# Kernel tuning notes

Measured on AMD Instinct MI355X. Metric: run time of the kernel, lower is better.

The kernel has to match this reference:

```python
import jax, jax.numpy as jnp
import numpy as np

N_ORDERS = 2
CHUNK = 64            # real tokens per chunk
LINEAR_ACTIVATION = False
STAB = 10000.0


def _ensure_stability(x):
    x = jnp.clip(x, -STAB, STAB)
    return jnp.nan_to_num(x, nan=0.0, posinf=STAB, neginf=-STAB)


def setup_inputs() -> dict:
    key = jax.random.key(0)
    k1, k2, k3, k4 = jax.random.split(key, 4)
    B, H, NC, D = 2, 16, 32, 128
    CT = CHUNK * N_ORDERS  # 128 virtual tokens per chunk
    s = 1.0 / np.sqrt(D)
    q_chunks = jax.random.normal(k1, (B, H, NC, CT, D), jnp.float32) * s
    W = jax.random.normal(k2, (B, H, NC, CT, D), jnp.float32) * s
    U = jax.random.normal(k3, (B, H, NC, CT, D), jnp.float32) * s
    h0 = jax.random.normal(k4, (B, H, D, D), jnp.float32) * s
    return {"q_chunks": q_chunks, "W": W, "U": U, "h0": h0}


def _gelu_norm(h):
    # h_norm/2 * gelu(2*h/h_norm, tanh) applied to chunk-boundary state
    n = jnp.linalg.norm(h, axis=-1, keepdims=True) + 1e-6
    return n / 2.0 * jax.nn.gelu(2.0 * h / n, approximate=True)


def _delta_product_scan(q_chunks, W, U, h0):
    B, H, NC, CT, D = q_chunks.shape
    C = CT // N_ORDERS

    def body(h, chunk):
        q_c, w_c, u_c = chunk  # each [B,H,CT,D]
        # virtual-token layout: token c, step s lives at index c*n_orders+s
        qs = q_c.reshape(B, H, C, N_ORDERS, D)
        ws = w_c.reshape(B, H, C, N_ORDERS, D)
        us = u_c.reshape(B, H, C, N_ORDERS, D)
        state = jnp.broadcast_to(h[:, :, None], (B, H, C, D, D))  # per-token state
        outs = []
        for step in range(N_ORDERS):
            q_s = qs[:, :, :, step]
            w_s = ws[:, :, :, step]
            u_s = us[:, :, :, step]
            k_trans_h = jnp.einsum('bhcd,bhcde->bhce', w_s, state)
            u_val = u_s - k_trans_h
            o_inter = jnp.einsum('bhcd,bhcde->bhce', q_s, state)
            o_intra = q_s * u_val  # elementwise, as in source
            outs.append(o_intra + o_inter)
            state = _ensure_stability(state + w_s[..., :, None] * u_val[..., None, :])
        out = jnp.stack(outs, axis=3).reshape(B, H, CT, D)
        h_new = state[:, :, -1]
        if not LINEAR_ACTIVATION:
            h_new = _gelu_norm(h_new)
        return h_new, out

    chunks = (jnp.moveaxis(q_chunks, 2, 0), jnp.moveaxis(W, 2, 0), jnp.moveaxis(U, 2, 0))
    h_final, ys = jax.lax.scan(body, h0, chunks)
    return jnp.moveaxis(ys, 0, 2), h_final  # [B,H,NC,CT,D], [B,H,D,D]


def reference(q_chunks, W, U, h0):
    return _delta_product_scan(q_chunks, W, U, h0)
```

## Files before the change

kernel.cpp:

```cpp
#include <hip/hip_runtime.h>


#define Dd 128
#define NCH 32
#define YS 16777216

typedef __attribute__((ext_vector_type(4))) float floatx4;
typedef __attribute__((ext_vector_type(8))) short short8;

__device__ __forceinline__ unsigned cvtpk(float lo, float hi) {
  unsigned r;
  asm("v_cvt_pk_bf16_f32 %0, %1, %2" : "=v"(r) : "v"(lo), "v"(hi));
  return r;
}

__global__ __launch_bounds__(512) void p1_scan(const float* __restrict__ W,
    const float* __restrict__ U, const float* __restrict__ h0,
    unsigned short* __restrict__ hws, float* __restrict__ out) {
  __shared__ float wpre[NCH * 320];
  __shared__ float upre[NCH * 2 * Dd];
  __shared__ float d10pre[NCH];
  __shared__ float sqb[Dd * 129];
  __shared__ float nrm2[4 * 40];

  const int bh = blockIdx.x;
  const int t = threadIdx.x;
  const int w = t >> 6, l = t & 63;
  const int c = (w << 4) | (l & 15);
  const int rg = l >> 4;

  {
    const float* Wg = W + (size_t)bh * NCH * 16384;
    const float* Ug = U + (size_t)bh * NCH * 16384;
#pragma unroll
    for (int k = 0; k < 4; k++) {
      int idx4 = k * 512 + t;
      int n = idx4 >> 6;
      int rem = idx4 & 63;
      int r = rem >> 5, e4 = (rem & 31) * 4;
      size_t g = (size_t)n * 16384 + (size_t)(126 + r) * Dd + e4;
      *(float4*)&upre[idx4 * 4] = *(const float4*)&Ug[g];
      *(float4*)&wpre[n * 320 + r * 160 + (e4 >> 5) * 40 + (e4 & 31)] =
          *(const float4*)&Wg[g];
    }
  }
  {
    const float4* hg = (const float4*)(h0 + (size_t)bh * 16384);
#pragma unroll
    for (int k = 0; k < 8; k++) {
      int idx4 = k * 512 + t;
      float4 v = hg[idx4];
      int d = idx4 >> 5, e4 = (idx4 & 31) * 4;
      sqb[d * 129 + e4 + 0] = v.x;
      sqb[d * 129 + e4 + 1] = v.y;
      sqb[d * 129 + e4 + 2] = v.z;
      sqb[d * 129 + e4 + 3] = v.w;
    }
  }
  __syncthreads();
  {
    int n = t >> 4, j = t & 15;
    const float* w0p = &wpre[n * 320 + (j >> 2) * 40 + (j & 3) * 8];
    const float* w1p = w0p + 160;
    float p = 0.f;
#pragma unroll
    for (int i = 0; i < 8; i++) p += w0p[i] * w1p[i];
    p += __shfl_xor(p, 1, 64);
    p += __shfl_xor(p, 2, 64);
    p += __shfl_xor(p, 4, 64);
    p += __shfl_xor(p, 8, 64);
    if (j == 0) d10pre[n] = p;
  }
  float hr[32];
#pragma unroll
  for (int i = 0; i < 32; i++) hr[i] = sqb[(rg * 32 + i) * 129 + c];
  __syncthreads();

  const int cpos = (c & 96) | ((c + 8 * rg) & 31);
  float* sqw = &sqb[rg * 32 * 129 + cpos];
  const int srow = t >> 2, sst = t & 3;
  const float* sqr = &sqb[srow * 129 + sst * 32];

  unsigned short* hwsb = hws + (size_t)bh * NCH * 16384;
  {
    unsigned pk[16];
#pragma unroll
    for (int i = 0; i < 16; i++) pk[i] = cvtpk(hr[2 * i], hr[2 * i + 1]);
    uint4* dst = (uint4*)(hwsb + (size_t)c * Dd + rg * 32);
    dst[0] = make_uint4(pk[0], pk[1], pk[2], pk[3]);
    dst[1] = make_uint4(pk[4], pk[5], pk[6], pk[7]);
    dst[2] = make_uint4(pk[8], pk[9], pk[10], pk[11]);
    dst[3] = make_uint4(pk[12], pk[13], pk[14], pk[15]);
  }

  for (int n = 0; n < NCH; n++) {
    floatx4 w0v[8], w1v[8];
    const float* wb = &wpre[n * 320 + rg * 40];
#pragma unroll
    for (int i = 0; i < 8; i++) {
      w0v[i] = *(const floatx4*)&wb[4 * i];
      w1v[i] = *(const floatx4*)&wb[160 + 4 * i];
    }
    float a0 = 0.f, a1 = 0.f, b0 = 0.f, b1 = 0.f;
#pragma unroll
    for (int i = 0; i < 8; i += 2) {
#pragma unroll
      for (int j = 0; j < 4; j++) {
        float h0v = hr[4 * i + j];
        float h1v = hr[4 * i + 4 + j];
        a0 = fmaf(w0v[i][j], h0v, a0);
        a1 = fmaf(w1v[i][j], h0v, a1);
        b0 = fmaf(w0v[i + 1][j], h1v, b0);
        b1 = fmaf(w1v[i + 1][j], h1v, b1);
      }
    }
    a0 += b0; a1 += b1;
    a0 += __shfl_xor(a0, 16, 64);
    a0 += __shfl_xor(a0, 32, 64);
    a1 += __shfl_xor(a1, 16, 64);
    a1 += __shfl_xor(a1, 32, 64);
    const float u0 = upre[n * 256 + c];
    const float u1 = upre[n * 256 + Dd + c];
    const float d10 = d10pre[n];
    const float uv0 = u0 - a0;
    const float uv1 = u1 - a1 - d10 * uv0;
#pragma unroll
    for (int i = 0; i < 8; i++)
#pragma unroll
      for (int j = 0; j < 4; j++) {
        int ii = 4 * i + j;
        float s = __builtin_amdgcn_fmed3f(fmaf(w0v[i][j], uv0, hr[ii]),
                                          -10000.0f, 10000.0f);
        s = __builtin_amdgcn_fmed3f(fmaf(w1v[i][j], uv1, s),
                                    -10000.0f, 10000.0f);
        hr[ii] = s;
        sqw[ii * 129] = s;
      }
    __syncthreads();
    {
      float acc = 0.f, acc2 = 0.f;
#pragma unroll
      for (int b = 0; b < 4; b++) {
        const float* p = sqr + 8 * ((b + sst) & 3);
#pragma unroll
        for (int i = 0; i < 8; i += 2) {
          float v = p[i], v2 = p[i + 1];
          acc = fmaf(v, v, acc);
          acc2 = fmaf(v2, v2, acc2);
        }
      }
      acc += acc2;
      acc += __shfl_xor(acc, 1, 64);
      acc += __shfl_xor(acc, 2, 64);
      if (sst == 0) {
        float nd = sqrtf(acc) + 1e-6f;
        nrm2[(srow >> 5) * 40 + (srow & 31)] = __fdividef(2.0f, nd);
      }
    }
    __syncthreads();
    floatx4 r2v[8];
    const float* nb = &nrm2[rg * 40];
#pragma unroll
    for (int i = 0; i < 8; i++) r2v[i] = *(const floatx4*)&nb[4 * i];
#pragma unroll
    for (int i = 0; i < 8; i++)
#pragma unroll
      for (int j = 0; j < 4; j++) {
        int ii = 4 * i + j;
        float h = hr[ii];
        float x = h * r2v[i][j];
        float x2 = x * x;
        float aa = x * fmaf(0.071354816f, x2, 1.59576912f);
        float ex = __expf(-aa);
        hr[ii] = __fdividef(h, 1.0f + ex);
      }
    if (n < NCH - 1) {
      unsigned pk[16];
#pragma unroll
      for (int i = 0; i < 16; i++) pk[i] = cvtpk(hr[2 * i], hr[2 * i + 1]);
      uint4* dst = (uint4*)(hwsb + (size_t)(n + 1) * 16384 + (size_t)c * Dd + rg * 32);
      dst[0] = make_uint4(pk[0], pk[1], pk[2], pk[3]);
      dst[1] = make_uint4(pk[4], pk[5], pk[6], pk[7]);
      dst[2] = make_uint4(pk[8], pk[9], pk[10], pk[11]);
      dst[3] = make_uint4(pk[12], pk[13], pk[14], pk[15]);
    } else {
      float* ob = out + YS + (size_t)bh * 16384;
#pragma unroll
      for (int i = 0; i < 32; i++) ob[(rg * 32 + i) * Dd + c] = hr[i];
    }
  }
}


__device__ __forceinline__ void stage_slice(const float* Qb, const float* Wb,
    float* qd, float* wd, int kc, int wv6, int ln) {
#pragma unroll
  for (int i = 0; i < 4; i++) {
    int cb = i * 512 + wv6 * 64;
    int isW = cb >> 10;
    int cbm = cb & 1023;
    int c = cbm + ln;
    int r = c >> 3;
    int s = (c >> 4) & 7;
    const float* g = (isW ? Wb : Qb) + r * Dd + kc * 32 + (((c & 7) ^ s) << 2);
    float* l = (isW ? wd : qd) + (cbm << 2);
    __builtin_amdgcn_global_load_lds(
        (const __attribute__((address_space(1))) void*)g,
        (__attribute__((address_space(3))) void*)l, 16, 0, 0);
  }
}

__global__ __launch_bounds__(512, 1) void p2_out(const float* __restrict__ Q,
    const float* __restrict__ W, const float* __restrict__ U,
    const unsigned short* __restrict__ hws, float* __restrict__ out) {
  __shared__ unsigned short hT[Dd * 136];
  __shared__ float qsl[2][4096];
  __shared__ float wsl[2][4096];
  __shared__ float d10s[64], dq1s[64];
  __shared__ float dps[512];

  const int bid = blockIdx.x;
  const int n = bid & 31, bh = bid >> 5;
  const size_t base = (size_t)(bh * NCH + n) * 16384;
  const float* Qb = Q + base;
  const float* Wb = W + base;
  const float* Ub = U + base;
  float* Ob = out + base;
  const int t = threadIdx.x;
  const int wv6 = t >> 6, ln = t & 63;

  stage_slice(Qb, Wb, &qsl[0][0], &wsl[0][0], 0, wv6, ln);

  {
    const uint4* src = (const uint4*)(hws + base);
#pragma unroll
    for (int i = 0; i < 4; i++) {
      int idx = t + i * 512;
      uint4 v = src[idx];
      int e = idx >> 4, j = idx & 15;
      *(uint4*)&hT[e * 136 + j * 8] = v;
    }
  }
  {
    int which = t >> 8, tt = t & 255;
    int cc = tt >> 2, part = tt & 3;
    const float4* ar = (const float4*)((which ? Qb : Wb) + (2 * cc + 1) * Dd + part * 32);
    const float4* w0r = (const float4*)(Wb + (2 * cc) * Dd + part * 32);
    float s = 0.f;
#pragma unroll
    for (int i = 0; i < 8; i++) {
      float4 a = ar[i], b = w0r[i];
      s += a.x * b.x + a.y * b.y + a.z * b.z + a.w * b.w;
    }
    dps[which * 256 + tt] = s;
  }
  __syncthreads();
  if (t < 128) {
    int which = t >> 6, cc = t & 63;
    const float* p = dps + which * 256 + cc * 4;
    float s = p[0] + p[1] + p[2] + p[3];
    (which ? dq1s : d10s)[cc] = s;
  }

  const int pr = wv6 >> 2, eq = wv6 & 3;
  const int lm = ln & 15, lq = ln >> 4;
  const int sw = lm & 7;
  const int i0 = ((2 * lq) ^ sw) << 2;
  const int i1 = ((2 * lq + 1) ^ sw) << 2;

  floatx4 acc[3][4][2];
#pragma unroll
  for (int m = 0; m < 3; m++)
#pragma unroll
    for (int ci = 0; ci < 4; ci++)
#pragma unroll
      for (int j = 0; j < 2; j++) acc[m][ci][j] = (floatx4){0.f, 0.f, 0.f, 0.f};

  int cur = 0;
  for (int kc = 0; kc < 4; kc++) {
    if (kc < 3)
      stage_slice(Qb, Wb, &qsl[cur ^ 1][0], &wsl[cur ^ 1][0], kc + 1, wv6, ln);
    const int k0 = kc * 32;
    short8 bfr[2];
#pragma unroll
    for (int j = 0; j < 2; j++) {
      int ee = (2 * eq + j) * 16 + lm;
      bfr[j] = *(const short8*)&hT[ee * 136 + k0 + 8 * lq];
    }
    const float* qs = &qsl[cur][0];
    const float* ws = &wsl[cur][0];
#pragma unroll
    for (int ci = 0; ci < 4; ci++) {
      const int rb = (32 * ci + 2 * lm) * 32;
      {
        const float* p = qs + rb + pr * 32;
        floatx4 g0 = *(const floatx4*)(p + i0);
        floatx4 g1 = *(const floatx4*)(p + i1);
        union { short8 v; unsigned u[4]; } af;
        af.u[0] = cvtpk(g0[0], g0[1]);
        af.u[1] = cvtpk(g0[2], g0[3]);
        af.u[2] = cvtpk(g1[0], g1[1]);
        af.u[3] = cvtpk(g1[2], g1[3]);
        acc[0][ci][0] = __builtin_amdgcn_mfma_f32_16x16x32_bf16(af.v, bfr[0], acc[0][ci][0], 0, 0, 0);
        acc[0][ci][1] = __builtin_amdgcn_mfma_f32_16x16x32_bf16(af.v, bfr[1], acc[0][ci][1], 0, 0, 0);
      }
      {
        const float* p = ws + rb + pr * 32;
        floatx4 g0 = *(const floatx4*)(p + i0);
        floatx4 g1 = *(const floatx4*)(p + i1);
        union { short8 v; unsigned u[4]; } af;
        af.u[0] = cvtpk(g0[0], g0[1]);
        af.u[1] = cvtpk(g0[2], g0[3]);
        af.u[2] = cvtpk(g1[0], g1[1]);
        af.u[3] = cvtpk(g1[2], g1[3]);
        acc[1][ci][0] = __builtin_amdgcn_mfma_f32_16x16x32_bf16(af.v, bfr[0], acc[1][ci][0], 0, 0, 0);
        acc[1][ci][1] = __builtin_amdgcn_mfma_f32_16x16x32_bf16(af.v, bfr[1], acc[1][ci][1], 0, 0, 0);
      }
      if (pr) {
        const float* p = ws + rb;
        floatx4 g0 = *(const floatx4*)(p + i0);
        floatx4 g1 = *(const floatx4*)(p + i1);
        union { short8 v; unsigned u[4]; } af;
        af.u[0] = cvtpk(g0[0], g0[1]);
        af.u[1] = cvtpk(g0[2], g0[3]);
        af.u[2] = cvtpk(g1[0], g1[1]);
        af.u[3] = cvtpk(g1[2], g1[3]);
        acc[2][ci][0] = __builtin_amdgcn_mfma_f32_16x16x32_bf16(af.v, bfr[0], acc[2][ci][0], 0, 0, 0);
        acc[2][ci][1] = __builtin_amdgcn_mfma_f32_16x16x32_bf16(af.v, bfr[1], acc[2][ci][1], 0, 0, 0);
      }
    }
    __syncthreads();
    cur ^= 1;
  }

  if (pr == 0) {
#pragma unroll
    for (int ci = 0; ci < 4; ci++)
#pragma unroll
      for (int j = 0; j < 2; j++) {
        int ee = (2 * eq + j) * 16 + lm;
#pragma unroll
        for (int r = 0; r < 4; r++) {
          int cc = ci * 16 + lq * 4 + r;
          float T0 = acc[1][ci][j][r];
          float Q0h = acc[0][ci][j][r];
          float u0 = Ub[(2 * cc) * Dd + ee];
          float q0 = Qb[(2 * cc) * Dd + ee];
          float uv0 = u0 - T0;
          Ob[(2 * cc) * Dd + ee] = q0 * uv0 + Q0h;
        }
      }
  } else {
#pragma unroll
    for (int ci = 0; ci < 4; ci++)
#pragma unroll
      for (int j = 0; j < 2; j++) {
        int ee = (2 * eq + j) * 16 + lm;
#pragma unroll
        for (int r = 0; r < 4; r++) {
          int cc = ci * 16 + lq * 4 + r;
          float T1 = acc[1][ci][j][r];
          float Q1h = acc[0][ci][j][r];
          float T0 = acc[2][ci][j][r];
          float u0 = Ub[(2 * cc) * Dd + ee];
          float u1 = Ub[(2 * cc + 1) * Dd + ee];
          float q1 = Qb[(2 * cc + 1) * Dd + ee];
          float uv0 = u0 - T0;
          float uv1 = u1 - T1 - d10s[cc] * uv0;
          Ob[(2 * cc + 1) * Dd + ee] = q1 * uv1 + Q1h + dq1s[cc] * uv0;
        }
      }
  }
}

extern "C" void kernel_launch(void* const* d_in, const int* in_sizes, int n_in,
                              void* d_out, int out_size, void* d_ws, size_t ws_size,
                              hipStream_t stream) {
  const float* Q = (const float*)d_in[0];
  const float* W = (const float*)d_in[1];
  const float* U = (const float*)d_in[2];
  const float* h0 = (const float*)d_in[3];
  float* out = (float*)d_out;
  unsigned short* hws = (unsigned short*)d_ws;

  p1_scan<<<32, 512, 0, stream>>>(W, U, h0, hws, out);
  p2_out<<<1024, 512, 0, stream>>>(Q, W, U, hws, out);
}
```

Measured before the change: 383.3 us.

## Use DPP row-norm reduction in scan; single-buffer p2 and share uv0 via LDS

In the scan kernel, the per-row squared norm is now reduced in registers with DPP row rotations and a small partial-sum buffer. This replaces writing the full state to shared memory and re-reading it. In the output kernel, the Q/W staging buffers drop from double to single buffering and launch bounds allow 4 blocks per CU. The redundant third MFMA accumulator is removed: uv0 is passed from the even-token waves to the odd-token waves through LDS (reusing hT), at the cost of an extra barrier. Single buffering gives up the overlap of loads with compute, betting that higher occupancy hides the latency instead.

```diff
diff --git a/kernel.cpp b/kernel.cpp
--- a/kernel.cpp
+++ b/kernel.cpp
@@ -13,6 +13,10 @@
   asm("v_cvt_pk_bf16_f32 %0, %1, %2" : "=v"(r) : "v"(lo), "v"(hi));
   return r;
 }
+
+#define ROTADD(p, CTRL)                                              \
+  p += __uint_as_float((unsigned)__builtin_amdgcn_update_dpp(        \
+      0, (int)__float_as_uint(p), (CTRL), 0xF, 0xF, false))
 
 __global__ __launch_bounds__(512) void p1_scan(const float* __restrict__ W,
     const float* __restrict__ U, const float* __restrict__ h0,
@@ -21,12 +25,14 @@
   __shared__ float upre[NCH * 2 * Dd];
   __shared__ float d10pre[NCH];
   __shared__ float sqb[Dd * 129];
+  __shared__ float ppart[8 * 132];
   __shared__ float nrm2[4 * 40];
 
   const int bh = blockIdx.x;
   const int t = threadIdx.x;
   const int w = t >> 6, l = t & 63;
-  const int c = (w << 4) | (l & 15);
+  const int cl = l & 15;
+  const int c = (w << 4) | cl;
   const int rg = l >> 4;
 
   {
@@ -75,11 +81,6 @@
 #pragma unroll
   for (int i = 0; i < 32; i++) hr[i] = sqb[(rg * 32 + i) * 129 + c];
   __syncthreads();
-
-  const int cpos = (c & 96) | ((c + 8 * rg) & 31);
-  float* sqw = &sqb[rg * 32 * 129 + cpos];
-  const int srow = t >> 2, sst = t & 3;
-  const float* sqr = &sqb[srow * 129 + sst * 32];
 
   unsigned short* hwsb = hws + (size_t)bh * NCH * 16384;
   {
@@ -134,28 +135,33 @@
         s = __builtin_amdgcn_fmed3f(fmaf(w1v[i][j], uv1, s),
                                     -10000.0f, 10000.0f);
         hr[ii] = s;
-        sqw[ii * 129] = s;
-      }
+      }
+    {
+      float r0s = 0.f, r1s = 0.f;
+#pragma unroll
+      for (int i = 0; i < 32; i++) {
+        float p = hr[i] * hr[i];
+        ROTADD(p, 0x128);
+        ROTADD(p, 0x124);
+        ROTADD(p, 0x122);
+        ROTADD(p, 0x121);
+        if (i < 16) r0s = (cl == i) ? p : r0s;
+        else        r1s = (cl == i - 16) ? p : r1s;
+      }
+      float* ppw = &ppart[w * 132 + rg * 32];
+      ppw[(cl + 13 * rg) & 31] = r0s;
+      ppw[(cl + 16 + 13 * rg) & 31] = r1s;
+    }
     __syncthreads();
-    {
-      float acc = 0.f, acc2 = 0.f;
-#pragma unroll
-      for (int b = 0; b < 4; b++) {
-        const float* p = sqr + 8 * ((b + sst) & 3);
-#pragma unroll
-        for (int i = 0; i < 8; i += 2) {
-          float v = p[i], v2 = p[i + 1];
-          acc = fmaf(v, v, acc);
-          acc2 = fmaf(v2, v2, acc2);
-        }
-      }
-      acc += acc2;
-      acc += __shfl_xor(acc, 1, 64);
-      acc += __shfl_xor(acc, 2, 64);
-      if (sst == 0) {
-        float nd = sqrtf(acc) + 1e-6f;
-        nrm2[(srow >> 5) * 40 + (srow & 31)] = __fdividef(2.0f, nd);
-      }
+    if (t < 128) {
+      int rgq = t >> 5, rr = t & 31;
+      int slot = rgq * 32 + ((rr + 13 * rgq) & 31);
+      float s = (ppart[slot] + ppart[132 + slot]) +
+                (ppart[264 + slot] + ppart[396 + slot]) +
+                (ppart[528 + slot] + ppart[660 + slot]) +
+                (ppart[792 + slot] + ppart[924 + slot]);
+      float nd = sqrtf(s) + 1e-6f;
+      nrm2[rgq * 40 + rr] = __fdividef(2.0f, nd);
     }
     __syncthreads();
     floatx4 r2v[8];
@@ -210,12 +216,12 @@
   }
 }
 
-__global__ __launch_bounds__(512, 1) void p2_out(const float* __restrict__ Q,
+__global__ __launch_bounds__(512, 4) void p2_out(const float* __restrict__ Q,
     const float* __restrict__ W, const float* __restrict__ U,
     const unsigned short* __restrict__ hws, float* __restrict__ out) {
   __shared__ unsigned short hT[Dd * 136];
-  __shared__ float qsl[2][4096];
-  __shared__ float wsl[2][4096];
+  __shared__ float qsl[4096];
+  __shared__ float wsl[4096];
   __shared__ float d10s[64], dq1s[64];
   __shared__ float dps[512];
 
@@ -229,7 +235,7 @@
   const int t = threadIdx.x;
   const int wv6 = t >> 6, ln = t & 63;
 
-  stage_slice(Qb, Wb, &qsl[0][0], &wsl[0][0], 0, wv6, ln);
+  stage_slice(Qb, Wb, &qsl[0], &wsl[0], 0, wv6, ln);
 
   {
     const uint4* src = (const uint4*)(hws + base);
@@ -268,18 +274,15 @@
   const int i0 = ((2 * lq) ^ sw) << 2;
   const int i1 = ((2 * lq + 1) ^ sw) << 2;
 
-  floatx4 acc[3][4][2];
-#pragma unroll
-  for (int m = 0; m < 3; m++)
+  floatx4 acc[2][4][2];
+#pragma unroll
+  for (int m = 0; m < 2; m++)
 #pragma unroll
     for (int ci = 0; ci < 4; ci++)
 #pragma unroll
       for (int j = 0; j < 2; j++) acc[m][ci][j] = (floatx4){0.f, 0.f, 0.f, 0.f};
 
-  int cur = 0;
   for (int kc = 0; kc < 4; kc++) {
-    if (kc < 3)
-      stage_slice(Qb, Wb, &qsl[cur ^ 1][0], &wsl[cur ^ 1][0], kc + 1, wv6, ln);
     const int k0 = kc * 32;
     short8 bfr[2];
 #pragma unroll
@@ -287,13 +290,11 @@
       int ee = (2 * eq + j) * 16 + lm;
       bfr[j] = *(const short8*)&hT[ee * 136 + k0 + 8 * lq];
     }
-    const float* qs = &qsl[cur][0];
-    const float* ws = &wsl[cur][0];
 #pragma unroll
     for (int ci = 0; ci < 4; ci++) {
-      const int rb = (32 * ci + 2 * lm) * 32;
+      const int rb = (32 * ci + 2 * lm) * 32 + pr * 32;
       {
-        const float* p = qs + rb + pr * 32;
+        const float* p = &qsl[rb];
         floatx4 g0 = *(const floatx4*)(p + i0);
         floatx4 g1 = *(const floatx4*)(p + i1);
         union { short8 v; unsigned u[4]; } af;
@@ -305,7 +306,7 @@
         acc[0][ci][1] = __builtin_amdgcn_mfma_f32_16x16x32_bf16(af.v, bfr[1], acc[0][ci][1], 0, 0, 0);
       }
       {
-        const float* p = ws + rb + pr * 32;
+        const float* p = &wsl[rb];
         floatx4 g0 = *(const floatx4*)(p + i0);
         floatx4 g1 = *(const floatx4*)(p + i1);
         union { short8 v; unsigned u[4]; } af;
@@ -316,23 +317,15 @@
         acc[1][ci][0] = __builtin_amdgcn_mfma_f32_16x16x32_bf16(af.v, bfr[0], acc[1][ci][0], 0, 0, 0);
         acc[1][ci][1] = __builtin_amdgcn_mfma_f32_16x16x32_bf16(af.v, bfr[1], acc[1][ci][1], 0, 0, 0);
       }
-      if (pr) {
-        const float* p = ws + rb;
-        floatx4 g0 = *(const floatx4*)(p + i0);
-        floatx4 g1 = *(const floatx4*)(p + i1);
-        union { short8 v; unsigned u[4]; } af;
-        af.u[0] = cvtpk(g0[0], g0[1]);
-        af.u[1] = cvtpk(g0[2], g0[3]);
-        af.u[2] = cvtpk(g1[0], g1[1]);
-        af.u[3] = cvtpk(g1[2], g1[3]);
-        acc[2][ci][0] = __builtin_amdgcn_mfma_f32_16x16x32_bf16(af.v, bfr[0], acc[2][ci][0], 0, 0, 0);
-        acc[2][ci][1] = __builtin_amdgcn_mfma_f32_16x16x32_bf16(af.v, bfr[1], acc[2][ci][1], 0, 0, 0);
-      }
     }
     __syncthreads();
-    cur ^= 1;
-  }
-
+    if (kc < 3) {
+      stage_slice(Qb, Wb, &qsl[0], &wsl[0], kc + 1, wv6, ln);
+      __syncthreads();
+    }
+  }
+
+  float* uv0s = (float*)hT;
   if (pr == 0) {
 #pragma unroll
     for (int ci = 0; ci < 4; ci++)
@@ -347,10 +340,13 @@
           float u0 = Ub[(2 * cc) * Dd + ee];
           float q0 = Qb[(2 * cc) * Dd + ee];
           float uv0 = u0 - T0;
+          uv0s[cc * Dd + ee] = uv0;
           Ob[(2 * cc) * Dd + ee] = q0 * uv0 + Q0h;
         }
       }
-  } else {
+  }
+  __syncthreads();
+  if (pr == 1) {
 #pragma unroll
     for (int ci = 0; ci < 4; ci++)
 #pragma unroll
@@ -361,11 +357,9 @@
           int cc = ci * 16 + lq * 4 + r;
           float T1 = acc[1][ci][j][r];
           float Q1h = acc[0][ci][j][r];
-          float T0 = acc[2][ci][j][r];
-          float u0 = Ub[(2 * cc) * Dd + ee];
           float u1 = Ub[(2 * cc + 1) * Dd + ee];
           float q1 = Qb[(2 * cc + 1) * Dd + ee];
-          float uv0 = u0 - T0;
+          float uv0 = uv0s[cc * Dd + ee];
           float uv1 = u1 - T1 - d10s[cc] * uv0;
           Ob[(2 * cc + 1) * Dd + ee] = q1 * uv1 + Q1h + dq1s[cc] * uv0;
         }
```

Result: slower. 394.1 us (+2.8%).
